# Kernel optimization log

Measured on AMD Instinct MI355X. Metric: run time of the kernel, lower is better.

## Reference

```python
import jax, jax.numpy as jnp
import numpy as np

N = 8192   # nodes
F = 16     # node features (col 0 = signal, last 3 = xyz)
H = 64     # hidden
G = 256    # number of graphs (segments)
EPS = 1e-3 # keras LayerNormalization default epsilon


def setup_inputs() -> dict:
    key = jax.random.key(0)
    ks = jax.random.split(key, 10)
    s = 0.05
    X = jax.random.normal(ks[0], (N, F), jnp.float32)
    # dense pre-normalized adjacency (spektral GCNConv expects normalized A)
    A = jax.random.uniform(ks[1], (N, N), jnp.float32) * (1.0 / N)
    I = jnp.sort(jax.random.randint(ks[2], (N,), 0, G)).astype(jnp.int32)
    W0 = jax.random.normal(ks[3], (F, H), jnp.float32) * s
    b0 = jnp.zeros((H,), jnp.float32)
    g0 = jnp.ones((H,), jnp.float32)
    be0 = jnp.zeros((H,), jnp.float32)
    W1 = jax.random.normal(ks[4], (H, H), jnp.float32) * s
    b1 = jnp.zeros((H,), jnp.float32)
    g1 = jnp.ones((H,), jnp.float32)
    be1 = jnp.zeros((H,), jnp.float32)
    Wf = jax.random.normal(ks[5], (H, H), jnp.float32) * s
    bf = jnp.zeros((H,), jnp.float32)
    Wa = jax.random.normal(ks[6], (H, H), jnp.float32) * s
    ba = jnp.zeros((H,), jnp.float32)
    Wout = jax.random.normal(ks[7], (H + 3, 3), jnp.float32) * s
    bout = jnp.zeros((3,), jnp.float32)
    return dict(X=X, A=A, I=I, W0=W0, b0=b0, g0=g0, be0=be0,
                W1=W1, b1=b1, g1=g1, be1=be1,
                Wf=Wf, bf=bf, Wa=Wa, ba=ba, Wout=Wout, bout=bout)


def _layer_norm(x, gamma, beta):
    m = jnp.mean(x, axis=-1, keepdims=True)
    v = jnp.mean(jnp.square(x - m), axis=-1, keepdims=True)
    return (x - m) * jax.lax.rsqrt(v + EPS) * gamma + beta


def reference(X, A, I, W0, b0, g0, be0, W1, b1, g1, be1, Wf, bf, Wa, ba, Wout, bout):
    I = I.astype(jnp.int32)
    # GCN layer 0: relu(A @ X @ W0 + b0) -> LayerNorm
    h0 = _layer_norm(jax.nn.relu(A @ (X @ W0) + b0), g0, be0)
    # GCN layer 1 + LayerNorm + residual (i > 0)
    h = _layer_norm(jax.nn.relu(A @ (h0 @ W1) + b1), g1, be1) + h0
    # GlobalAttentionPool: Dense features * sigmoid-gated attention, segment-summed per graph
    feat = h @ Wf + bf                       # [N, H]
    attn = jax.nn.sigmoid(h @ Wa + ba)       # [N, H]
    g = jax.ops.segment_sum(feat * attn, I, num_segments=G)  # [G, H]
    # Signal-weighted barycentre via segment-softmax over log1p(relu(signal))
    z = jnp.log1p(jax.nn.relu(X[:, 0]))                       # [N]
    zmax = jax.ops.segment_max(z, I, num_segments=G)          # [G]
    zexp = jnp.exp(z - zmax[I])                               # [N]
    zsum = jax.ops.segment_sum(zexp, I, num_segments=G)       # [G]
    w = zexp / zsum[I]                                        # [N]
    bary = jax.ops.segment_sum(w[:, None] * X[:, -3:], I, num_segments=G)  # [G, 3]
    return jnp.concatenate([g, bary], axis=-1) @ Wout + bout  # [G, 3]
```

## Files before the change

kernel.cpp:

```cpp
#include <hip/hip_runtime.h>
#include <hip/hip_bf16.h>
#include <math.h>

#define NN 8192
#define FF 16
#define HH 64
#define GG 256
#define LN_EPS 1e-3f
#define BK 256
#define KSTAGES (NN / BK)

typedef __bf16 bf16x8 __attribute__((ext_vector_type(8)));
typedef float  floatx4 __attribute__((ext_vector_type(4)));

__global__ __launch_bounds__(256)
void k1_xw0(const float* __restrict__ X,
            const float* __restrict__ W0,
            const int* __restrict__ I,
            __hip_bfloat16* __restrict__ Zt0,
            float* __restrict__ zarr,
            unsigned int* __restrict__ zmax_bits) {
    __shared__ float Xs[64][17];
    __shared__ float W0s[16][64];
    const int t  = threadIdx.x;
    const int i0 = blockIdx.x * 64;
    {
        const int r = t >> 2, c = (t & 3) * 4;
        const float4 v = *reinterpret_cast<const float4*>(&X[(size_t)(i0 + r) * FF + c]);
        Xs[r][c + 0] = v.x; Xs[r][c + 1] = v.y; Xs[r][c + 2] = v.z; Xs[r][c + 3] = v.w;
        const float4 w = *reinterpret_cast<const float4*>(&W0[t * 4]);
        const int wr = t >> 4, wc = (t & 15) * 4;
        W0s[wr][wc + 0] = w.x; W0s[wr][wc + 1] = w.y; W0s[wr][wc + 2] = w.z; W0s[wr][wc + 3] = w.w;
    }
    __syncthreads();
    const int i  = t & 63;
    const int n0 = (t >> 6) * 16;
    float s[16];
#pragma unroll
    for (int j = 0; j < 16; ++j) s[j] = 0.f;
#pragma unroll
    for (int m = 0; m < FF; ++m) {
        const float hv = Xs[i][m];
        const float4* wrow = reinterpret_cast<const float4*>(&W0s[m][n0]);
        const float4 w0 = wrow[0], w1 = wrow[1], w2 = wrow[2], w3 = wrow[3];
        s[0]  += hv * w0.x; s[1]  += hv * w0.y; s[2]  += hv * w0.z; s[3]  += hv * w0.w;
        s[4]  += hv * w1.x; s[5]  += hv * w1.y; s[6]  += hv * w1.z; s[7]  += hv * w1.w;
        s[8]  += hv * w2.x; s[9]  += hv * w2.y; s[10] += hv * w2.z; s[11] += hv * w2.w;
        s[12] += hv * w3.x; s[13] += hv * w3.y; s[14] += hv * w3.z; s[15] += hv * w3.w;
    }
#pragma unroll
    for (int j = 0; j < 16; ++j)
        Zt0[(size_t)(n0 + j) * NN + i0 + i] = __float2bfloat16(s[j]);

    if (t < 64) {
        const float z = log1pf(fmaxf(Xs[t][0], 0.f));
        zarr[i0 + t] = z;
        atomicMax(&zmax_bits[I[i0 + t]], __float_as_uint(z));
    }
}

__global__ __launch_bounds__(256)
void k_gemm_lds(const float* __restrict__ A,
                const __hip_bfloat16* __restrict__ Zt,
                float* __restrict__ C) {
    __shared__ float Ab[2][16][256];
    const int t    = threadIdx.x;
    const int w    = t >> 6;
    const int lane = t & 63;
    const int l16  = lane & 15;
    const int quad = lane >> 4;
    const int row0 = blockIdx.x * 16;
    const int sc   = lane * 4;
    const int swz  = (l16 & 7) << 2;

    const __hip_bfloat16* bp = Zt + (size_t)(w * 16 + l16) * NN + quad * 8;
    const float* arow = A + (size_t)row0 * NN;

    floatx4 acc = {0.f, 0.f, 0.f, 0.f};

    {
        float4 st[4];
#pragma unroll
        for (int j = 0; j < 4; ++j)
            st[j] = *reinterpret_cast<const float4*>(arow + (size_t)(j * 4 + w) * NN + sc);
#pragma unroll
        for (int j = 0; j < 4; ++j) {
            const int r = j * 4 + w;
            *reinterpret_cast<float4*>(&Ab[0][r][sc ^ ((r & 7) << 2)]) = st[j];
        }
    }
    __syncthreads();

    int cur = 0;
    for (int s = 0; s < KSTAGES; ++s) {
        float4 nx[4];
        const bool pf = (s + 1 < KSTAGES);
        if (pf) {
#pragma unroll
            for (int j = 0; j < 4; ++j)
                nx[j] = *reinterpret_cast<const float4*>(
                    arow + (size_t)(j * 4 + w) * NN + (size_t)(s + 1) * BK + sc);
        }
#pragma unroll
        for (int kk = 0; kk < 8; ++kk) {
            const int c = kk * 32 + quad * 8;
            const float4 alo = *reinterpret_cast<const float4*>(&Ab[cur][l16][(c    ) ^ swz]);
            const float4 ahi = *reinterpret_cast<const float4*>(&Ab[cur][l16][(c + 4) ^ swz]);
            bf16x8 af;
            af[0]=(__bf16)alo.x; af[1]=(__bf16)alo.y; af[2]=(__bf16)alo.z; af[3]=(__bf16)alo.w;
            af[4]=(__bf16)ahi.x; af[5]=(__bf16)ahi.y; af[6]=(__bf16)ahi.z; af[7]=(__bf16)ahi.w;
            const bf16x8 b = *reinterpret_cast<const bf16x8*>(bp + (size_t)s * BK + kk * 32);
            acc = __builtin_amdgcn_mfma_f32_16x16x32_bf16(af, b, acc, 0, 0, 0);
        }
        if (pf) {
#pragma unroll
            for (int j = 0; j < 4; ++j) {
                const int r = j * 4 + w;
                *reinterpret_cast<float4*>(&Ab[cur ^ 1][r][sc ^ ((r & 7) << 2)]) = nx[j];
            }
        }
        __syncthreads();
        cur ^= 1;
    }

#pragma unroll
    for (int r = 0; r < 4; ++r)
        C[(size_t)(row0 + quad * 4 + r) * HH + w * 16 + l16] = acc[r];
}

__global__ __launch_bounds__(256)
void k_ln(const float* __restrict__ C,
          const float* __restrict__ bias,
          const float* __restrict__ gamma,
          const float* __restrict__ beta,
          const float* __restrict__ resid,
          float* __restrict__ out) {
    const int tid = threadIdx.x;
    const int row = tid >> 4;
    const int c0  = (tid & 15) * 4;
    const size_t grow = (size_t)(blockIdx.x * 16 + row);

    const float4 a = *reinterpret_cast<const float4*>(&C[grow * HH + c0]);
    const float4 b4 = *reinterpret_cast<const float4*>(&bias[c0]);
    float v[4] = { fmaxf(a.x + b4.x, 0.f), fmaxf(a.y + b4.y, 0.f),
                   fmaxf(a.z + b4.z, 0.f), fmaxf(a.w + b4.w, 0.f) };
    float s = 0.f, ss = 0.f;
#pragma unroll
    for (int j = 0; j < 4; ++j) { s += v[j]; ss += v[j] * v[j]; }
#pragma unroll
    for (int m = 1; m < 16; m <<= 1) {
        s  += __shfl_xor(s,  m, 64);
        ss += __shfl_xor(ss, m, 64);
    }
    const float mean = s * (1.f / 64.f);
    const float var  = fmaxf(ss * (1.f / 64.f) - mean * mean, 0.f);
    const float inv  = rsqrtf(var + LN_EPS);
    const float4 g4  = *reinterpret_cast<const float4*>(&gamma[c0]);
    const float4 be4 = *reinterpret_cast<const float4*>(&beta[c0]);
    float4 o;
    o.x = (v[0] - mean) * inv * g4.x + be4.x;
    o.y = (v[1] - mean) * inv * g4.y + be4.y;
    o.z = (v[2] - mean) * inv * g4.z + be4.z;
    o.w = (v[3] - mean) * inv * g4.w + be4.w;
    if (resid) {
        const float4 r4 = *reinterpret_cast<const float4*>(&resid[grow * HH + c0]);
        o.x += r4.x; o.y += r4.y; o.z += r4.z; o.w += r4.w;
    }
    *reinterpret_cast<float4*>(&out[grow * HH + c0]) = o;
}

__global__ __launch_bounds__(256)
void k3_hw1(const float* __restrict__ h0,
            const float* __restrict__ W1,
            __hip_bfloat16* __restrict__ Zt1) {
    __shared__ float Hs[64][65];
    __shared__ float Ws[64][64];
    const int t  = threadIdx.x;
    const int i0 = blockIdx.x * 64;
#pragma unroll
    for (int p = 0; p < 4; ++p) {
        const int idx = p * 256 + t;
        const int r = idx >> 4, c = (idx & 15) * 4;
        const float4 v = *reinterpret_cast<const float4*>(&h0[(size_t)(i0 + r) * HH + c]);
        Hs[r][c + 0] = v.x; Hs[r][c + 1] = v.y; Hs[r][c + 2] = v.z; Hs[r][c + 3] = v.w;
        const float4 w = *reinterpret_cast<const float4*>(&W1[(size_t)r * HH + c]);
        Ws[r][c + 0] = w.x; Ws[r][c + 1] = w.y; Ws[r][c + 2] = w.z; Ws[r][c + 3] = w.w;
    }
    __syncthreads();
    const int i  = t & 63;
    const int n0 = (t >> 6) * 16;
    float s[16];
#pragma unroll
    for (int j = 0; j < 16; ++j) s[j] = 0.f;
#pragma unroll
    for (int m = 0; m < HH; ++m) {
        const float hv = Hs[i][m];
        const float4* wrow = reinterpret_cast<const float4*>(&Ws[m][n0]);
        const float4 w0 = wrow[0], w1 = wrow[1], w2 = wrow[2], w3 = wrow[3];
        s[0]  += hv * w0.x; s[1]  += hv * w0.y; s[2]  += hv * w0.z; s[3]  += hv * w0.w;
        s[4]  += hv * w1.x; s[5]  += hv * w1.y; s[6]  += hv * w1.z; s[7]  += hv * w1.w;
        s[8]  += hv * w2.x; s[9]  += hv * w2.y; s[10] += hv * w2.z; s[11] += hv * w2.w;
        s[12] += hv * w3.x; s[13] += hv * w3.y; s[14] += hv * w3.z; s[15] += hv * w3.w;
    }
#pragma unroll
    for (int j = 0; j < 16; ++j)
        Zt1[(size_t)(n0 + j) * NN + i0 + i] = __float2bfloat16(s[j]);
}

__global__ __launch_bounds__(256)
void k5_pool(const float* __restrict__ h,
             const float* __restrict__ Wf, const float* __restrict__ bfv,
             const float* __restrict__ Wa, const float* __restrict__ bav,
             const int* __restrict__ I,
             const float* __restrict__ X,
             const float* __restrict__ zarr,
             const float* __restrict__ zmax,
             float* __restrict__ g,
             float* __restrict__ zsum,
             float* __restrict__ baryn) {
    __shared__ float hrow[4][64];
    const int w = threadIdx.x >> 6, l = threadIdx.x & 63;
    const int node = blockIdx.x * 4 + w;
    hrow[w][l] = h[(size_t)node * HH + l];
    __syncthreads();
    float sf = bfv[l], sa = bav[l];
#pragma unroll 8
    for (int m = 0; m < HH; ++m) {
        const float hv = hrow[w][m];
        sf += hv * Wf[m * HH + l];
        sa += hv * Wa[m * HH + l];
    }
    const float attn = 1.f / (1.f + expf(-sa));
    const int seg = I[node];
    atomicAdd(&g[(size_t)seg * HH + l], sf * attn);

    if (l < 4) {
        const float ze = expf(zarr[node] - zmax[seg]);
        if (l == 0) atomicAdd(&zsum[seg], ze);
        else        atomicAdd(&baryn[seg * 3 + (l - 1)], ze * X[(size_t)node * FF + 12 + l]);
    }
}

__global__ __launch_bounds__(256)
void k7_out(const float* __restrict__ g,
            const float* __restrict__ zsum,
            const float* __restrict__ baryn,
            const float* __restrict__ Wout,
            const float* __restrict__ bout,
            float* __restrict__ out) {
    const int w = threadIdx.x >> 6, lane = threadIdx.x & 63;
    const int gi = blockIdx.x * 4 + w;
    const float vg = g[(size_t)gi * HH + lane];
    const float zs = zsum[gi];
    const float invz = (zs > 0.f) ? (1.f / zs) : 0.f;
    const float extra = (lane < 3) ? baryn[gi * 3 + lane] * invz : 0.f;
#pragma unroll
    for (int d = 0; d < 3; ++d) {
        float p = vg * Wout[lane * 3 + d];
        if (lane < 3) p += extra * Wout[(64 + lane) * 3 + d];
#pragma unroll
        for (int m = 1; m < 64; m <<= 1) p += __shfl_xor(p, m, 64);
        if (lane == 0) out[gi * 3 + d] = p + bout[d];
    }
}

extern "C" void kernel_launch(void* const* d_in, const int* in_sizes, int n_in,
                              void* d_out, int out_size, void* d_ws, size_t ws_size,
                              hipStream_t stream) {
    const float* X   = (const float*)d_in[0];
    const float* A   = (const float*)d_in[1];
    const int*   I   = (const int*)d_in[2];
    const float* W0  = (const float*)d_in[3];
    const float* b0  = (const float*)d_in[4];
    const float* g0  = (const float*)d_in[5];
    const float* be0 = (const float*)d_in[6];
    const float* W1  = (const float*)d_in[7];
    const float* b1  = (const float*)d_in[8];
    const float* g1  = (const float*)d_in[9];
    const float* be1 = (const float*)d_in[10];
    const float* Wf  = (const float*)d_in[11];
    const float* bfv = (const float*)d_in[12];
    const float* Wa  = (const float*)d_in[13];
    const float* bav = (const float*)d_in[14];
    const float* Wo  = (const float*)d_in[15];
    const float* bo  = (const float*)d_in[16];

    char* ws = (char*)d_ws;
    float* C    = (float*)ws;
    __hip_bfloat16* Zt0 = (__hip_bfloat16*)(ws + (2u << 20));
    __hip_bfloat16* Zt1 = (__hip_bfloat16*)(ws + (3u << 20));
    float* h0   = (float*)(ws + (4u << 20));
    float* h    = (float*)(ws + (6u << 20));
    float* zarr = (float*)(ws + (8u << 20));
    float* acc  = (float*)(ws + (8u << 20) + (64u << 10));
    float* g     = acc;
    float* zmax  = acc + GG * HH;
    float* zsum  = zmax + GG;
    float* baryn = zsum + GG;
    const size_t memset_bytes = (size_t)(GG * HH + GG + GG + GG * 3) * sizeof(float);

    hipMemsetAsync(acc, 0, memset_bytes, stream);

    k1_xw0<<<128, 256, 0, stream>>>(X, W0, I, Zt0, zarr, (unsigned int*)zmax);
    k_gemm_lds<<<512, 256, 0, stream>>>(A, Zt0, C);
    k_ln<<<512, 256, 0, stream>>>(C, b0, g0, be0, nullptr, h0);
    k3_hw1<<<128, 256, 0, stream>>>(h0, W1, Zt1);
    k_gemm_lds<<<512, 256, 0, stream>>>(A, Zt1, C);
    k_ln<<<512, 256, 0, stream>>>(C, b1, g1, be1, h0, h);
    k5_pool<<<2048, 256, 0, stream>>>(h, Wf, bfv, Wa, bav, I, X, zarr, zmax, g, zsum, baryn);
    k7_out<<<64, 256, 0, stream>>>(g, zsum, baryn, Wo, bo, (float*)d_out);
}
```

Before: 684.0 us.

## Fuse LayerNorm into GEMM, stage A as bf16 in LDS with larger K tile

Merges the A@Z GEMM with the bias/ReLU/LayerNorm epilogue, so the intermediate C matrix is no longer written to and re-read from global memory and two kernel launches go away. The A tile is now converted to bf16 once when it is written to LDS, instead of being converted on every fragment read. The K tile grows from 256 to 1024 with 16 float4 prefetch registers per thread. The larger register footprint and LDS use may cut occupancy in this memory-bound kernel, which streams the 256MB A matrix.

Result: faster. 561.9 us (-17.9%).

```diff
diff --git a/kernel.cpp b/kernel.cpp
--- a/kernel.cpp
+++ b/kernel.cpp
@@ -7,8 +7,8 @@
 #define HH 64
 #define GG 256
 #define LN_EPS 1e-3f
-#define BK 256
-#define KSTAGES (NN / BK)
+#define BK 1024
+#define NST (NN / BK)
 
 typedef __bf16 bf16x8 __attribute__((ext_vector_type(8)));
 typedef float  floatx4 __attribute__((ext_vector_type(4)));
@@ -60,90 +60,107 @@
 }
 
 __global__ __launch_bounds__(256)
-void k_gemm_lds(const float* __restrict__ A,
-                const __hip_bfloat16* __restrict__ Zt,
-                float* __restrict__ C) {
-    __shared__ float Ab[2][16][256];
+void k_gemm_ln(const float* __restrict__ A,
+               const __hip_bfloat16* __restrict__ Zt,
+               const float* __restrict__ bias,
+               const float* __restrict__ gamma,
+               const float* __restrict__ beta,
+               const float* __restrict__ resid,
+               float* __restrict__ out) {
+    __shared__ __hip_bfloat16 Ab[2][16][BK];
+    __shared__ float CLn[16][68];
     const int t    = threadIdx.x;
     const int w    = t >> 6;
     const int lane = t & 63;
     const int l16  = lane & 15;
     const int quad = lane >> 4;
     const int row0 = blockIdx.x * 16;
-    const int sc   = lane * 4;
-    const int swz  = (l16 & 7) << 2;
 
     const __hip_bfloat16* bp = Zt + (size_t)(w * 16 + l16) * NN + quad * 8;
     const float* arow = A + (size_t)row0 * NN;
 
+    char* ab0 = reinterpret_cast<char*>(&Ab[0][0][0]);
+    char* ab1 = reinterpret_cast<char*>(&Ab[1][0][0]);
+
     floatx4 acc = {0.f, 0.f, 0.f, 0.f};
 
+#define STAGE_LOAD(dst, s_)                                                      \
+    {                                                                            \
+        _Pragma("unroll")                                                        \
+        for (int r4 = 0; r4 < 4; ++r4)                                           \
+            _Pragma("unroll")                                                    \
+            for (int c = 0; c < 4; ++c)                                          \
+                dst[r4 * 4 + c] = *reinterpret_cast<const float4*>(              \
+                    arow + (size_t)(w * 4 + r4) * NN + (size_t)(s_) * BK +       \
+                    c * 256 + lane * 4);                                         \
+    }
+#define STAGE_WRITE(src, abase)                                                  \
+    {                                                                            \
+        _Pragma("unroll")                                                        \
+        for (int r4 = 0; r4 < 4; ++r4) {                                         \
+            const int row = w * 4 + r4;                                          \
+            const int rsw = (row & 7) << 4;                                      \
+            _Pragma("unroll")                                                    \
+            for (int c = 0; c < 4; ++c) {                                        \
+                const float4 v = src[r4 * 4 + c];                                \
+                __hip_bfloat16 h0_ = __float2bfloat16(v.x);                      \
+                __hip_bfloat16 h1_ = __float2bfloat16(v.y);                      \
+                __hip_bfloat16 h2_ = __float2bfloat16(v.z);                      \
+                __hip_bfloat16 h3_ = __float2bfloat16(v.w);                      \
+                ushort4 u;                                                       \
+                u.x = *reinterpret_cast<unsigned short*>(&h0_);                  \
+                u.y = *reinterpret_cast<unsigned short*>(&h1_);                  \
+                u.z = *reinterpret_cast<unsigned short*>(&h2_);                  \
+                u.w = *reinterpret_cast<unsigned short*>(&h3_);                  \
+                const int cbyte = (c * 256 + lane * 4) * 2;                      \
+                *reinterpret_cast<ushort4*>(                                     \
+                    abase + row * (BK * 2) + (cbyte ^ rsw)) = u;                 \
+            }                                                                    \
+        }                                                                        \
+    }
+
     {
-        float4 st[4];
-#pragma unroll
-        for (int j = 0; j < 4; ++j)
-            st[j] = *reinterpret_cast<const float4*>(arow + (size_t)(j * 4 + w) * NN + sc);
-#pragma unroll
-        for (int j = 0; j < 4; ++j) {
-            const int r = j * 4 + w;
-            *reinterpret_cast<float4*>(&Ab[0][r][sc ^ ((r & 7) << 2)]) = st[j];
-        }
-    }
-    __syncthreads();
-
+        float4 st[16];
+        STAGE_LOAD(st, 0)
+        STAGE_WRITE(st, ab0)
+    }
+    __syncthreads();
+
+    const int rswz = (l16 & 7) << 4;
     int cur = 0;
-    for (int s = 0; s < KSTAGES; ++s) {
-        float4 nx[4];
-        const bool pf = (s + 1 < KSTAGES);
-        if (pf) {
-#pragma unroll
-            for (int j = 0; j < 4; ++j)
-                nx[j] = *reinterpret_cast<const float4*>(
-                    arow + (size_t)(j * 4 + w) * NN + (size_t)(s + 1) * BK + sc);
-        }
-#pragma unroll
-        for (int kk = 0; kk < 8; ++kk) {
-            const int c = kk * 32 + quad * 8;
-            const float4 alo = *reinterpret_cast<const float4*>(&Ab[cur][l16][(c    ) ^ swz]);
-            const float4 ahi = *reinterpret_cast<const float4*>(&Ab[cur][l16][(c + 4) ^ swz]);
-            bf16x8 af;
-            af[0]=(__bf16)alo.x; af[1]=(__bf16)alo.y; af[2]=(__bf16)alo.z; af[3]=(__bf16)alo.w;
-            af[4]=(__bf16)ahi.x; af[5]=(__bf16)ahi.y; af[6]=(__bf16)ahi.z; af[7]=(__bf16)ahi.w;
-            const bf16x8 b = *reinterpret_cast<const bf16x8*>(bp + (size_t)s * BK + kk * 32);
+    for (int s = 0; s < NST; ++s) {
+        float4 nx[16];
+        const bool pf = (s + 1 < NST);
+        if (pf) STAGE_LOAD(nx, s + 1)
+        const char* ab = cur ? ab1 : ab0;
+        const char* arow_l = ab + l16 * (BK * 2);
+#pragma unroll 4
+        for (int kk = 0; kk < BK / 32; ++kk) {
+            const bf16x8 af = *reinterpret_cast<const bf16x8*>(
+                arow_l + ((kk * 64 + quad * 16) ^ rswz));
+            const bf16x8 b = *reinterpret_cast<const bf16x8*>(
+                bp + (size_t)s * BK + kk * 32);
             acc = __builtin_amdgcn_mfma_f32_16x16x32_bf16(af, b, acc, 0, 0, 0);
         }
-        if (pf) {
-#pragma unroll
-            for (int j = 0; j < 4; ++j) {
-                const int r = j * 4 + w;
-                *reinterpret_cast<float4*>(&Ab[cur ^ 1][r][sc ^ ((r & 7) << 2)]) = nx[j];
-            }
-        }
+        if (pf) STAGE_WRITE(nx, (cur ? ab0 : ab1))
         __syncthreads();
         cur ^= 1;
     }
+#undef STAGE_LOAD
+#undef STAGE_WRITE
 
 #pragma unroll
     for (int r = 0; r < 4; ++r)
-        C[(size_t)(row0 + quad * 4 + r) * HH + w * 16 + l16] = acc[r];
-}
-
-__global__ __launch_bounds__(256)
-void k_ln(const float* __restrict__ C,
-          const float* __restrict__ bias,
-          const float* __restrict__ gamma,
-          const float* __restrict__ beta,
-          const float* __restrict__ resid,
-          float* __restrict__ out) {
-    const int tid = threadIdx.x;
-    const int row = tid >> 4;
-    const int c0  = (tid & 15) * 4;
-    const size_t grow = (size_t)(blockIdx.x * 16 + row);
-
-    const float4 a = *reinterpret_cast<const float4*>(&C[grow * HH + c0]);
+        CLn[quad * 4 + r][w * 16 + l16] = acc[r];
+    __syncthreads();
+
+    const int row = t >> 4;
+    const int c0  = (t & 15) * 4;
+    const size_t grow = (size_t)(row0 + row);
+    const float4 a4 = *reinterpret_cast<const float4*>(&CLn[row][c0]);
     const float4 b4 = *reinterpret_cast<const float4*>(&bias[c0]);
-    float v[4] = { fmaxf(a.x + b4.x, 0.f), fmaxf(a.y + b4.y, 0.f),
-                   fmaxf(a.z + b4.z, 0.f), fmaxf(a.w + b4.w, 0.f) };
+    float v[4] = { fmaxf(a4.x + b4.x, 0.f), fmaxf(a4.y + b4.y, 0.f),
+                   fmaxf(a4.z + b4.z, 0.f), fmaxf(a4.w + b4.w, 0.f) };
     float s = 0.f, ss = 0.f;
 #pragma unroll
     for (int j = 0; j < 4; ++j) { s += v[j]; ss += v[j] * v[j]; }
@@ -286,13 +303,12 @@
     const float* bo  = (const float*)d_in[16];
 
     char* ws = (char*)d_ws;
-    float* C    = (float*)ws;
-    __hip_bfloat16* Zt0 = (__hip_bfloat16*)(ws + (2u << 20));
-    __hip_bfloat16* Zt1 = (__hip_bfloat16*)(ws + (3u << 20));
-    float* h0   = (float*)(ws + (4u << 20));
-    float* h    = (float*)(ws + (6u << 20));
-    float* zarr = (float*)(ws + (8u << 20));
-    float* acc  = (float*)(ws + (8u << 20) + (64u << 10));
+    __hip_bfloat16* Zt0 = (__hip_bfloat16*)(ws);
+    __hip_bfloat16* Zt1 = (__hip_bfloat16*)(ws + (1u << 20));
+    float* h0   = (float*)(ws + (2u << 20));
+    float* h    = (float*)(ws + (4u << 20));
+    float* zarr = (float*)(ws + (6u << 20));
+    float* acc  = (float*)(ws + (6u << 20) + (64u << 10));
     float* g     = acc;
     float* zmax  = acc + GG * HH;
     float* zsum  = zmax + GG;
@@ -302,11 +318,9 @@
     hipMemsetAsync(acc, 0, memset_bytes, stream);
 
     k1_xw0<<<128, 256, 0, stream>>>(X, W0, I, Zt0, zarr, (unsigned int*)zmax);
-    k_gemm_lds<<<512, 256, 0, stream>>>(A, Zt0, C);
-    k_ln<<<512, 256, 0, stream>>>(C, b0, g0, be0, nullptr, h0);
+    k_gemm_ln<<<512, 256, 0, stream>>>(A, Zt0, b0, g0, be0, nullptr, h0);
     k3_hw1<<<128, 256, 0, stream>>>(h0, W1, Zt1);
-    k_gemm_lds<<<512, 256, 0, stream>>>(A, Zt1, C);
-    k_ln<<<512, 256, 0, stream>>>(C, b1, g1, be1, h0, h);
+    k_gemm_ln<<<512, 256, 0, stream>>>(A, Zt1, b1, g1, be1, h0, h);
     k5_pool<<<2048, 256, 0, stream>>>(h, Wf, bfv, Wa, bav, I, X, zarr, zmax, g, zsum, baryn);
     k7_out<<<64, 256, 0, stream>>>(g, zsum, baryn, Wo, bo, (float*)d_out);
 }
```
